# Kernel optimization log

Measured on AMD Instinct MI355X. Metric: run time of the kernel, lower is better.

Reference implementation:

```python
import jax, jax.numpy as jnp
import numpy as np

B, L, DIN, H, E, K = 64, 256, 768, 64, 8, 2
S = 16  # sqrt(L): token<->feature grid side
LOSS_COEF = 1e-2


def gelu(x):
    return jax.nn.gelu(x, approximate=False)  # torch nn.GELU (exact erf)


def cv_squared(v):
    v = v.astype(jnp.float32)
    return jnp.var(v, ddof=1) / (jnp.mean(v) ** 2 + 1e-10)


def setup_inputs() -> dict:
    key = jax.random.key(0)
    ks = jax.random.split(key, 16)
    rn = lambda k, shape, s=0.02: jax.random.normal(k, shape, jnp.float32) * s
    lap = jnp.array([[0., 1., 0.], [1., -4., 1.], [0., 1., 0.]], jnp.float32)
    return {
        "x": jax.random.normal(ks[0], (B, L, DIN), jnp.float32),
        "dte": jax.random.normal(ks[1], (B, L, DIN), jnp.float32),
        "w_gate": rn(ks[2], (L, E), 1.0),
        "W_exp": rn(ks[3], (E, DIN, H)), "b_exp": jnp.zeros((E, H), jnp.float32),
        "W_sh": rn(ks[4], (DIN, H)), "b_sh": jnp.zeros((H,), jnp.float32),
        "ln_g": jnp.ones((H,), jnp.float32), "ln_b": jnp.zeros((H,), jnp.float32),
        "W_px": rn(ks[5], (H, 2 * H)), "b_px": jnp.zeros((2 * H,), jnp.float32),
        "conv_sh": jnp.tile(lap[None, None], (H, 1, 1, 1)),  # depthwise Laplacian [H,1,3,3]
        "W_pxx": rn(ks[6], (H, H)), "b_pxx": jnp.zeros((H,), jnp.float32),
        "W_dte": rn(ks[7], (H, H)), "b_dte": jnp.zeros((H,), jnp.float32),
        "W_dteall": rn(ks[8], (H, H)), "b_dteall": jnp.zeros((H,), jnp.float32),
        "W_rgb": rn(ks[9], (DIN, H)), "b_rgb": jnp.zeros((H,), jnp.float32),
        "W_fx": rn(ks[10], (H, H)), "b_fx": jnp.zeros((H,), jnp.float32),
        "W_fmod": rn(ks[11], (H, H)), "b_fmod": jnp.zeros((H,), jnp.float32),
        "W_fxx": rn(ks[12], (H, H)), "b_fxx": jnp.zeros((H,), jnp.float32),
    }


def reference(x, dte, w_gate, W_exp, b_exp, W_sh, b_sh, ln_g, ln_b, W_px, b_px,
              conv_sh, W_pxx, b_pxx, W_dte, b_dte, W_dteall, b_dteall,
              W_rgb, b_rgb, W_fx, b_fx, W_fmod, b_fmod, W_fxx, b_fxx):
    # ---- top-k gating (clean logits; noisy_gating=False / eval) ----
    logits = dte.mean(-1) @ w_gate                     # [B,E]
    topv, topi = jax.lax.top_k(logits, K)
    topg = jax.nn.softmax(topv, axis=1)
    gates = jnp.zeros_like(logits).at[jnp.arange(B)[:, None], topi].set(topg)
    importance = gates.sum(0)
    load = (gates > 0).sum(0).astype(jnp.float32)
    loss = LOSS_COEF * (cv_squared(importance) + cv_squared(load))
    # ---- sparse dispatch / expert Linear / weighted combine (dense-equivalent) ----
    y = jnp.einsum('be,bld,edh->blh', gates, dte, W_exp) + (gates @ b_exp)[:, None, :]
    # ---- shared expert Linear + Shared block ----
    sh = dte @ W_sh + b_sh                             # [B,L,H]
    shortcut = sh
    t = (sh - sh.mean(-1, keepdims=True)) * jax.lax.rsqrt(sh.var(-1, keepdims=True) + 1e-6)
    t = t * ln_g + ln_b
    t = t @ W_px + b_px                                # [B,L,2H]
    t1, t2 = t[..., :H], t[..., H:]
    f = t1.transpose(0, 2, 1).reshape(B, H, S, S)      # token2feature
    f = jax.lax.conv_general_dilated(f, conv_sh, (1, 1), 'SAME', feature_group_count=H)
    t1 = f.reshape(B, H, L).transpose(0, 2, 1)         # feature2token
    sh = (gelu(t1) * t2) @ W_pxx + b_pxx + shortcut
    # ---- combine MoE and shared streams ----
    dte_tok = (y @ W_dte + b_dte) + (sh @ W_dteall + b_dteall)
    rgb_tok = x @ W_rgb + b_rgb
    # ---- Fusion (its self.norm was overwritten to GELU; token<->feature round-trip is identity) ----
    shortcut = rgb_tok
    a = gelu(rgb_tok) @ W_fx + b_fx
    m = gelu(dte_tok) @ W_fmod + b_fmod
    out = (gelu(m) * a) @ W_fxx + b_fxx + shortcut     # [B,L,H]
    return out, loss
```

## Files before the change

kernel.cpp:

```cpp
#include <hip/hip_runtime.h>
#include <math.h>

typedef unsigned short u16;
typedef unsigned int u32;
typedef __attribute__((ext_vector_type(8))) short bf16x8;
typedef __attribute__((ext_vector_type(4))) float f32x4;


__device__ __forceinline__ float bf2f(u16 u) {
    union { u32 i; float f; } x; x.i = ((u32)u) << 16; return x.f;
}
__device__ __forceinline__ u16 f2bf(float f) {
    union { float f; u32 i; } x; x.f = f;
    u32 i = x.i;
    return (u16)((i + 0x7fffu + ((i >> 16) & 1u)) >> 16);
}
__device__ __forceinline__ u32 pack2(float a, float b) {
    return (u32)f2bf(a) | ((u32)f2bf(b) << 16);
}
__device__ __forceinline__ float wsum(float v) {
    #pragma unroll
    for (int o = 1; o < 64; o <<= 1) v += __shfl_xor(v, o, 64);
    return v;
}
__device__ __forceinline__ float gelu_f(float x) {
    return 0.5f * x * (1.0f + erff(x * 0.70710678118654752440f));
}

__global__ __launch_bounds__(256) void k_gate_part(const float* __restrict__ dte,
                                                   const float* __restrict__ w_gate,
                                                   float* __restrict__ partial) {
    __shared__ float dmeanS[64];
    int p = blockIdx.x, tid = threadIdx.x, w = tid >> 6, lane = tid & 63;
    for (int i = 0; i < 16; i++) {
        int l = w * 16 + i;
        const float* pr = dte + ((size_t)p * 64 + l) * 768;
        float s = 0.f;
        #pragma unroll
        for (int j = 0; j < 3; j++) {
            float4 v = *(const float4*)(pr + (lane + j * 64) * 4);
            s += v.x + v.y + v.z + v.w;
        }
        s = wsum(s);
        if (lane == 0) dmeanS[l] = s * (1.f / 768.f);
    }
    __syncthreads();
    if (w == 0) {
        float dm = dmeanS[lane];
        int wl = (p & 3) * 64 + lane;
        #pragma unroll
        for (int e = 0; e < 8; e++) {
            float s = wsum(dm * w_gate[wl * 8 + e]);
            if (lane == 0) partial[p * 8 + e] = s;
        }
    }
}

__global__ __launch_bounds__(256) void k_gate_fin(const float* __restrict__ partial,
                                                  const float* __restrict__ b_exp,
                                                  int* __restrict__ topi,
                                                  float* __restrict__ topg,
                                                  float* __restrict__ bias_y,
                                                  float* __restrict__ loss_out) {
    __shared__ float gS[64 * 8];
    __shared__ int i0S[64], i1S[64];
    __shared__ float g0S[64], g1S[64];
    int tid = threadIdx.x;
    if (tid < 64) {
        float lg[8];
        #pragma unroll
        for (int e = 0; e < 8; e++)
            lg[e] = partial[(tid * 4 + 0) * 8 + e] + partial[(tid * 4 + 1) * 8 + e] +
                    partial[(tid * 4 + 2) * 8 + e] + partial[(tid * 4 + 3) * 8 + e];
        int i0 = 0; float v0 = lg[0];
        #pragma unroll
        for (int e = 1; e < 8; e++) if (lg[e] > v0) { v0 = lg[e]; i0 = e; }
        int i1 = -1; float v1 = -1e30f;
        #pragma unroll
        for (int e = 0; e < 8; e++) if (e != i0 && lg[e] > v1) { v1 = lg[e]; i1 = e; }
        if (i1 < 0) i1 = (i0 + 1) & 7;
        float e2 = expf(v1 - v0);
        float g0 = 1.f / (1.f + e2);
        float g1 = e2 / (1.f + e2);
        #pragma unroll
        for (int e = 0; e < 8; e++) gS[tid * 8 + e] = 0.f;
        gS[tid * 8 + i0] = g0;
        gS[tid * 8 + i1] = g1;
        i0S[tid] = i0; i1S[tid] = i1; g0S[tid] = g0; g1S[tid] = g1;
        topi[tid * 2] = i0; topi[tid * 2 + 1] = i1;
        topg[tid * 2] = g0; topg[tid * 2 + 1] = g1;
    }
    __syncthreads();
    for (int idx = tid; idx < 4096; idx += 256) {
        int b = idx >> 6, h = idx & 63;
        bias_y[idx] = g0S[b] * b_exp[i0S[b] * 64 + h] + g1S[b] * b_exp[i1S[b] * 64 + h];
    }
    if (tid < 64) {
        float g[8];
        #pragma unroll
        for (int e = 0; e < 8; e++) g[e] = gS[tid * 8 + e];
        float imp[8], ld[8];
        #pragma unroll
        for (int e = 0; e < 8; e++) {
            imp[e] = wsum(g[e]);
            ld[e]  = wsum(g[e] > 0.f ? 1.f : 0.f);
        }
        if (tid == 0) {
            float l = 0.f;
            {
                float s = 0.f;
                #pragma unroll
                for (int e = 0; e < 8; e++) s += imp[e];
                float mn = s / 8.f, v = 0.f;
                #pragma unroll
                for (int e = 0; e < 8; e++) { float d = imp[e] - mn; v += d * d; }
                l += (v / 7.f) / (mn * mn + 1e-10f);
            }
            {
                float s = 0.f;
                #pragma unroll
                for (int e = 0; e < 8; e++) s += ld[e];
                float mn = s / 8.f, v = 0.f;
                #pragma unroll
                for (int e = 0; e < 8; e++) { float d = ld[e] - mn; v += d * d; }
                l += (v / 7.f) / (mn * mn + 1e-10f);
            }
            loss_out[0] = 0.01f * l;
        }
    }
}

__global__ __launch_bounds__(256) void k_gemm3(const float* __restrict__ dte,
                                               const float* __restrict__ x,
                                               const float* __restrict__ W_sh,
                                               const float* __restrict__ b_sh,
                                               const float* __restrict__ W_exp,
                                               const int* __restrict__ topi,
                                               const float* __restrict__ topg,
                                               const float* __restrict__ bias_y,
                                               const float* __restrict__ W_rgb,
                                               const float* __restrict__ b_rgb,
                                               float* __restrict__ buf_sh,
                                               u16* __restrict__ buf_y,
                                               float* __restrict__ out_rgb) {
    __shared__ u16 As[64 * 40];
    __shared__ u16 Wt[64 * 40];
    int bid = blockIdx.x;
    int kind, row0;
    if (bid < 512) { kind = bid & 1; row0 = (bid >> 1) * 64; }
    else           { kind = 2;       row0 = (bid - 512) * 64; }
    int b = row0 >> 8;
    int tid = threadIdx.x, wv = tid >> 6, lane = tid & 63;
    int m = lane & 15, quad = lane >> 4;

    const float* A = (kind == 2) ? x : dte;
    const float* W0 = (kind == 2) ? W_rgb : W_sh;
    const float* W1 = W0;
    float g0 = 0.f, g1 = 0.f;
    if (kind == 1) {
        W0 = W_exp + (size_t)topi[2 * b] * 49152;
        W1 = W_exp + (size_t)topi[2 * b + 1] * 49152;
        g0 = topg[2 * b]; g1 = topg[2 * b + 1];
    }

    f32x4 acc0 = {0.f, 0.f, 0.f, 0.f}, acc1 = acc0, acc2 = acc0, acc3 = acc0;

    for (int kc = 0; kc < 24; kc++) {
        __syncthreads();
        #pragma unroll
        for (int j = 0; j < 2; j++) {
            int e4 = tid + j * 256;
            int r = e4 >> 3, kq = e4 & 7;
            float4 v = *(const float4*)(A + (size_t)(row0 + r) * 768 + kc * 32 + kq * 4);
            u32* d = (u32*)&As[r * 40 + kq * 4];
            d[0] = pack2(v.x, v.y);
            d[1] = pack2(v.z, v.w);
        }
        #pragma unroll
        for (int j = 0; j < 2; j++) {
            int e4 = tid + j * 256;
            int k = e4 >> 4, n4 = (e4 & 15) * 4;
            size_t off = (size_t)(kc * 32 + k) * 64 + n4;
            float4 wvv;
            if (kind == 1) {
                float4 a = *(const float4*)(W0 + off);
                float4 c = *(const float4*)(W1 + off);
                wvv.x = g0 * a.x + g1 * c.x; wvv.y = g0 * a.y + g1 * c.y;
                wvv.z = g0 * a.z + g1 * c.z; wvv.w = g0 * a.w + g1 * c.w;
            } else {
                wvv = *(const float4*)(W0 + off);
            }
            Wt[(n4 + 0) * 40 + k] = f2bf(wvv.x);
            Wt[(n4 + 1) * 40 + k] = f2bf(wvv.y);
            Wt[(n4 + 2) * 40 + k] = f2bf(wvv.z);
            Wt[(n4 + 3) * 40 + k] = f2bf(wvv.w);
        }
        __syncthreads();
        bf16x8 a = *(const bf16x8*)&As[(wv * 16 + m) * 40 + quad * 8];
        bf16x8 b0 = *(const bf16x8*)&Wt[(0 * 16 + m) * 40 + quad * 8];
        bf16x8 b1 = *(const bf16x8*)&Wt[(1 * 16 + m) * 40 + quad * 8];
        bf16x8 b2 = *(const bf16x8*)&Wt[(2 * 16 + m) * 40 + quad * 8];
        bf16x8 b3 = *(const bf16x8*)&Wt[(3 * 16 + m) * 40 + quad * 8];
        acc0 = __builtin_amdgcn_mfma_f32_16x16x32_bf16(a, b0, acc0, 0, 0, 0);
        acc1 = __builtin_amdgcn_mfma_f32_16x16x32_bf16(a, b1, acc1, 0, 0, 0);
        acc2 = __builtin_amdgcn_mfma_f32_16x16x32_bf16(a, b2, acc2, 0, 0, 0);
        acc3 = __builtin_amdgcn_mfma_f32_16x16x32_bf16(a, b3, acc3, 0, 0, 0);
    }

    f32x4 accs[4] = {acc0, acc1, acc2, acc3};
    #pragma unroll
    for (int t = 0; t < 4; t++) {
        int col = t * 16 + m;
        float bias;
        if (kind == 0)      bias = b_sh[col];
        else if (kind == 1) bias = bias_y[b * 64 + col];
        else                bias = b_rgb[col];
        #pragma unroll
        for (int i = 0; i < 4; i++) {
            int r = row0 + wv * 16 + quad * 4 + i;
            float val = accs[t][i] + bias;
            if (kind == 0)      buf_sh[(size_t)r * 64 + col] = val;
            else if (kind == 1) buf_y[(size_t)r * 64 + col] = f2bf(val);
            else                out_rgb[(size_t)r * 64 + col] = val;
        }
    }
}

__global__ __launch_bounds__(256) void k_lnpx(const float* __restrict__ buf_sh,
                                              const float* __restrict__ ln_g,
                                              const float* __restrict__ ln_b,
                                              const float* __restrict__ W_px,
                                              const float* __restrict__ b_px,
                                              u16* __restrict__ t1, u16* __restrict__ t2) {
    __shared__ float T[32 * 68];
    __shared__ float Wpx[8192];
    int r0 = blockIdx.x * 32;
    int tid = threadIdx.x, w = tid >> 6, lane = tid & 63;
    #pragma unroll
    for (int j = 0; j < 8; j++) {
        int e4 = tid + j * 256;
        *(float4*)(Wpx + e4 * 4) = *(const float4*)(W_px + e4 * 4);
    }
    float lnG = ln_g[lane], lnB = ln_b[lane];
    for (int i = 0; i < 8; i++) {
        int l = w * 8 + i;
        float v = buf_sh[(size_t)(r0 + l) * 64 + lane];
        float mean = wsum(v) * (1.f / 64.f);
        float d = v - mean;
        float var = wsum(d * d) * (1.f / 64.f);
        T[l * 68 + lane] = d * rsqrtf(var + 1e-6f) * lnG + lnB;
    }
    __syncthreads();
    int rg = tid >> 4, cg = tid & 15;
    float acc1[2][4] = {}, acc2[2][4] = {};
    const float* tr = T + rg * 2 * 68;
    #pragma unroll 4
    for (int kk = 0; kk < 64; kk++) {
        float a0 = tr[kk], a1 = tr[68 + kk];
        float4 w1 = *(const float4*)(Wpx + kk * 128 + cg * 4);
        float4 w2 = *(const float4*)(Wpx + kk * 128 + 64 + cg * 4);
        acc1[0][0] += a0 * w1.x; acc1[0][1] += a0 * w1.y; acc1[0][2] += a0 * w1.z; acc1[0][3] += a0 * w1.w;
        acc1[1][0] += a1 * w1.x; acc1[1][1] += a1 * w1.y; acc1[1][2] += a1 * w1.z; acc1[1][3] += a1 * w1.w;
        acc2[0][0] += a0 * w2.x; acc2[0][1] += a0 * w2.y; acc2[0][2] += a0 * w2.z; acc2[0][3] += a0 * w2.w;
        acc2[1][0] += a1 * w2.x; acc2[1][1] += a1 * w2.y; acc2[1][2] += a1 * w2.z; acc2[1][3] += a1 * w2.w;
    }
    float4 b1 = *(const float4*)(b_px + cg * 4);
    float4 b2 = *(const float4*)(b_px + 64 + cg * 4);
    #pragma unroll
    for (int i = 0; i < 2; i++) {
        int r = r0 + rg * 2 + i;
        u32* d1 = (u32*)(t1 + (size_t)r * 64 + cg * 4);
        d1[0] = pack2(acc1[i][0] + b1.x, acc1[i][1] + b1.y);
        d1[1] = pack2(acc1[i][2] + b1.z, acc1[i][3] + b1.w);
        u32* d2 = (u32*)(t2 + (size_t)r * 64 + cg * 4);
        d2[0] = pack2(acc2[i][0] + b2.x, acc2[i][1] + b2.y);
        d2[1] = pack2(acc2[i][2] + b2.z, acc2[i][3] + b2.w);
    }
}

__global__ __launch_bounds__(256) void k_tail(const u16* __restrict__ t1,
                                              const u16* __restrict__ t2,
                                              const float* __restrict__ conv_sh,
                                              const float* __restrict__ W_pxx,
                                              const float* __restrict__ b_pxx,
                                              const float* __restrict__ buf_sh,
                                              const u16* __restrict__ buf_y,
                                              const float* __restrict__ W_dte,
                                              const float* __restrict__ b_dte,
                                              const float* __restrict__ W_dteall,
                                              const float* __restrict__ b_dteall,
                                              const float* __restrict__ W_fx,
                                              const float* __restrict__ b_fx,
                                              const float* __restrict__ W_fmod,
                                              const float* __restrict__ b_fmod,
                                              const float* __restrict__ W_fxx,
                                              const float* __restrict__ b_fxx,
                                              float* __restrict__ out) {
    __shared__ float B0[32 * 68];
    __shared__ float B1[32 * 68];
    __shared__ float B2[32 * 68];
    __shared__ float RS[32 * 64];
    int r0 = blockIdx.x * 32;
    int tid = threadIdx.x, w = tid >> 6, lane = tid & 63;
    int rg = tid >> 4, cg = tid & 15;

    {
        float c0 = conv_sh[lane * 9 + 0], c1 = conv_sh[lane * 9 + 1], c2 = conv_sh[lane * 9 + 2];
        float c3 = conv_sh[lane * 9 + 3], c4 = conv_sh[lane * 9 + 4], c5 = conv_sh[lane * 9 + 5];
        float c6 = conv_sh[lane * 9 + 6], c7 = conv_sh[lane * 9 + 7], c8 = conv_sh[lane * 9 + 8];
        for (int i = 0; i < 8; i++) {
            int l = w * 8 + i;
            int gr = r0 + l;
            int pix = gr & 255, ii = pix >> 4, jj = pix & 15;
            const u16* p = t1 + (size_t)gr * 64 + lane;
            float c = c4 * bf2f(p[0]);
            if (ii > 0) {
                c += c1 * bf2f(p[-1024]);
                if (jj > 0)  c += c0 * bf2f(p[-1024 - 64]);
                if (jj < 15) c += c2 * bf2f(p[-1024 + 64]);
            }
            if (jj > 0)  c += c3 * bf2f(p[-64]);
            if (jj < 15) c += c5 * bf2f(p[64]);
            if (ii < 15) {
                c += c7 * bf2f(p[1024]);
                if (jj > 0)  c += c6 * bf2f(p[1024 - 64]);
                if (jj < 15) c += c8 * bf2f(p[1024 + 64]);
            }
            B0[l * 68 + lane] = gelu_f(c) * bf2f(t2[(size_t)gr * 64 + lane]);
        }
    }
    __syncthreads();

    {
        float acc[2][4] = {};
        const float* ur = B0 + rg * 2 * 68;
        #pragma unroll 8
        for (int kk = 0; kk < 64; kk++) {
            float a0 = ur[kk], a1 = ur[68 + kk];
            float4 wvv = *(const float4*)(W_pxx + kk * 64 + cg * 4);
            acc[0][0] += a0 * wvv.x; acc[0][1] += a0 * wvv.y; acc[0][2] += a0 * wvv.z; acc[0][3] += a0 * wvv.w;
            acc[1][0] += a1 * wvv.x; acc[1][1] += a1 * wvv.y; acc[1][2] += a1 * wvv.z; acc[1][3] += a1 * wvv.w;
        }
        float4 bp = *(const float4*)(b_pxx + cg * 4);
        #pragma unroll
        for (int i = 0; i < 2; i++) {
            int lr = rg * 2 + i;
            float4 shv = *(const float4*)(buf_sh + (size_t)(r0 + lr) * 64 + cg * 4);
            *(float4*)(B1 + lr * 68 + cg * 4) =
                make_float4(acc[i][0] + bp.x + shv.x, acc[i][1] + bp.y + shv.y,
                            acc[i][2] + bp.z + shv.z, acc[i][3] + bp.w + shv.w);
        }
    }
    __syncthreads();

    #pragma unroll
    for (int j = 0; j < 8; j++) {
        int e = tid + j * 256;
        int l = e >> 6, c = e & 63;
        B0[l * 68 + c] = bf2f(buf_y[(size_t)(r0 + l) * 64 + c]);
    }
    __syncthreads();

    {
        float acc[2][4] = {};
        const float* yr = B0 + rg * 2 * 68;
        const float* sr = B1 + rg * 2 * 68;
        #pragma unroll 4
        for (int kk = 0; kk < 64; kk++) {
            float y0 = yr[kk], y1 = yr[68 + kk];
            float s0 = sr[kk], s1 = sr[68 + kk];
            float4 w1 = *(const float4*)(W_dte + kk * 64 + cg * 4);
            float4 w2 = *(const float4*)(W_dteall + kk * 64 + cg * 4);
            acc[0][0] += y0 * w1.x + s0 * w2.x; acc[0][1] += y0 * w1.y + s0 * w2.y;
            acc[0][2] += y0 * w1.z + s0 * w2.z; acc[0][3] += y0 * w1.w + s0 * w2.w;
            acc[1][0] += y1 * w1.x + s1 * w2.x; acc[1][1] += y1 * w1.y + s1 * w2.y;
            acc[1][2] += y1 * w1.z + s1 * w2.z; acc[1][3] += y1 * w1.w + s1 * w2.w;
        }
        float4 bd1 = *(const float4*)(b_dte + cg * 4);
        float4 bd2 = *(const float4*)(b_dteall + cg * 4);
        #pragma unroll
        for (int i = 0; i < 2; i++) {
            int lr = rg * 2 + i;
            *(float4*)(B2 + lr * 68 + cg * 4) =
                make_float4(gelu_f(acc[i][0] + bd1.x + bd2.x), gelu_f(acc[i][1] + bd1.y + bd2.y),
                            gelu_f(acc[i][2] + bd1.z + bd2.z), gelu_f(acc[i][3] + bd1.w + bd2.w));
        }
    }
    __syncthreads();

    #pragma unroll
    for (int j = 0; j < 2; j++) {
        int e4 = tid + j * 256;
        int l = e4 >> 4, c4i = e4 & 15;
        float4 rv = *(const float4*)(out + (size_t)(r0 + l) * 64 + c4i * 4);
        *(float4*)(RS + l * 64 + c4i * 4) = rv;
        B1[l * 68 + c4i * 4 + 0] = gelu_f(rv.x);
        B1[l * 68 + c4i * 4 + 1] = gelu_f(rv.y);
        B1[l * 68 + c4i * 4 + 2] = gelu_f(rv.z);
        B1[l * 68 + c4i * 4 + 3] = gelu_f(rv.w);
    }
    __syncthreads();

    {
        float accA[2][4] = {}, accM[2][4] = {};
        const float* ga = B1 + rg * 2 * 68;
        const float* gm = B2 + rg * 2 * 68;
        #pragma unroll 4
        for (int kk = 0; kk < 64; kk++) {
            float a0 = ga[kk], a1 = ga[68 + kk];
            float m0 = gm[kk], m1 = gm[68 + kk];
            float4 wa = *(const float4*)(W_fx + kk * 64 + cg * 4);
            float4 wm = *(const float4*)(W_fmod + kk * 64 + cg * 4);
            accA[0][0] += a0 * wa.x; accA[0][1] += a0 * wa.y; accA[0][2] += a0 * wa.z; accA[0][3] += a0 * wa.w;
            accA[1][0] += a1 * wa.x; accA[1][1] += a1 * wa.y; accA[1][2] += a1 * wa.z; accA[1][3] += a1 * wa.w;
            accM[0][0] += m0 * wm.x; accM[0][1] += m0 * wm.y; accM[0][2] += m0 * wm.z; accM[0][3] += m0 * wm.w;
            accM[1][0] += m1 * wm.x; accM[1][1] += m1 * wm.y; accM[1][2] += m1 * wm.z; accM[1][3] += m1 * wm.w;
        }
        float4 bx = *(const float4*)(b_fx + cg * 4);
        float4 bm = *(const float4*)(b_fmod + cg * 4);
        #pragma unroll
        for (int i = 0; i < 2; i++) {
            int lr = rg * 2 + i;
            float a0 = accA[i][0] + bx.x, a1 = accA[i][1] + bx.y, a2 = accA[i][2] + bx.z, a3 = accA[i][3] + bx.w;
            float m0 = accM[i][0] + bm.x, m1 = accM[i][1] + bm.y, m2 = accM[i][2] + bm.z, m3 = accM[i][3] + bm.w;
            *(float4*)(B0 + lr * 68 + cg * 4) =
                make_float4(gelu_f(m0) * a0, gelu_f(m1) * a1, gelu_f(m2) * a2, gelu_f(m3) * a3);
        }
    }
    __syncthreads();

    {
        float acc[2][4] = {};
        const float* pr = B0 + rg * 2 * 68;
        #pragma unroll 8
        for (int kk = 0; kk < 64; kk++) {
            float p0 = pr[kk], p1 = pr[68 + kk];
            float4 wvv = *(const float4*)(W_fxx + kk * 64 + cg * 4);
            acc[0][0] += p0 * wvv.x; acc[0][1] += p0 * wvv.y; acc[0][2] += p0 * wvv.z; acc[0][3] += p0 * wvv.w;
            acc[1][0] += p1 * wvv.x; acc[1][1] += p1 * wvv.y; acc[1][2] += p1 * wvv.z; acc[1][3] += p1 * wvv.w;
        }
        float4 bo = *(const float4*)(b_fxx + cg * 4);
        #pragma unroll
        for (int i = 0; i < 2; i++) {
            int lr = rg * 2 + i;
            *(float4*)(out + (size_t)(r0 + lr) * 64 + cg * 4) =
                make_float4(acc[i][0] + bo.x + RS[lr * 64 + cg * 4 + 0],
                            acc[i][1] + bo.y + RS[lr * 64 + cg * 4 + 1],
                            acc[i][2] + bo.z + RS[lr * 64 + cg * 4 + 2],
                            acc[i][3] + bo.w + RS[lr * 64 + cg * 4 + 3]);
        }
    }
}

extern "C" void kernel_launch(void* const* d_in, const int* in_sizes, int n_in,
                              void* d_out, int out_size, void* d_ws, size_t ws_size,
                              hipStream_t stream) {
    const float* x       = (const float*)d_in[0];
    const float* dte     = (const float*)d_in[1];
    const float* w_gate  = (const float*)d_in[2];
    const float* W_exp   = (const float*)d_in[3];
    const float* b_exp   = (const float*)d_in[4];
    const float* W_sh    = (const float*)d_in[5];
    const float* b_sh    = (const float*)d_in[6];
    const float* ln_g    = (const float*)d_in[7];
    const float* ln_b    = (const float*)d_in[8];
    const float* W_px    = (const float*)d_in[9];
    const float* b_px    = (const float*)d_in[10];
    const float* conv_sh = (const float*)d_in[11];
    const float* W_pxx   = (const float*)d_in[12];
    const float* b_pxx   = (const float*)d_in[13];
    const float* W_dte   = (const float*)d_in[14];
    const float* b_dte   = (const float*)d_in[15];
    const float* W_dteall= (const float*)d_in[16];
    const float* b_dteall= (const float*)d_in[17];
    const float* W_rgb   = (const float*)d_in[18];
    const float* b_rgb   = (const float*)d_in[19];
    const float* W_fx    = (const float*)d_in[20];
    const float* b_fx    = (const float*)d_in[21];
    const float* W_fmod  = (const float*)d_in[22];
    const float* b_fmod  = (const float*)d_in[23];
    const float* W_fxx   = (const float*)d_in[24];
    const float* b_fxx   = (const float*)d_in[25];

    float* out = (float*)d_out;

    float* wsf    = (float*)d_ws;
    float* partial= wsf;
    int*   topi   = (int*)(wsf + 2048);
    float* topg   = wsf + 2176;
    float* bias_y = wsf + 2304;
    float* buf_sh = wsf + 8192;
    u16*   buf_y  = (u16*)(wsf + 8192 + 1048576);
    u16*   t1     = (u16*)(wsf + 8192 + 1048576 + 524288);
    u16*   t2     = (u16*)(wsf + 8192 + 1048576 + 524288*2);

    hipLaunchKernelGGL(k_gate_part, dim3(256), dim3(256), 0, stream, dte, w_gate, partial);
    hipLaunchKernelGGL(k_gate_fin, dim3(1), dim3(256), 0, stream,
                       partial, b_exp, topi, topg, bias_y, out + 1048576);
    hipLaunchKernelGGL(k_gemm3, dim3(768), dim3(256), 0, stream,
                       dte, x, W_sh, b_sh, W_exp, topi, topg, bias_y, W_rgb, b_rgb,
                       buf_sh, buf_y, out);
    hipLaunchKernelGGL(k_lnpx, dim3(512), dim3(256), 0, stream,
                       buf_sh, ln_g, ln_b, W_px, b_px, t1, t2);
    hipLaunchKernelGGL(k_tail, dim3(512), dim3(256), 0, stream,
                       t1, t2, conv_sh, W_pxx, b_pxx, buf_sh, buf_y,
                       W_dte, b_dte, W_dteall, b_dteall,
                       W_fx, b_fx, W_fmod, b_fmod, W_fxx, b_fxx, out);

    (void)in_sizes; (void)n_in; (void)out_size; (void)ws_size;
}
```

Baseline: 278.7 us.

## Prefetch next K-chunk into registers and double the K tile in gemm3

The main projection GEMM kernel now loads the next K chunk from global memory into registers while the MFMAs for the current chunk run, so global latency overlaps compute. The K tile grows from 32 to 64, which halves the number of barrier pairs, and the weight tile is now written transposed with 16-byte vector LDS stores instead of scalar stores. The cost is more registers per thread (prefetch buffers) and larger LDS tiles. The weight loads also become scalar but coalesced per column.

```diff
diff --git a/kernel.cpp b/kernel.cpp
--- a/kernel.cpp
+++ b/kernel.cpp
@@ -143,8 +143,8 @@
                                                float* __restrict__ buf_sh,
                                                u16* __restrict__ buf_y,
                                                float* __restrict__ out_rgb) {
-    __shared__ u16 As[64 * 40];
-    __shared__ u16 Wt[64 * 40];
+    __shared__ u16 As[64 * 72];
+    __shared__ u16 Wt[64 * 72];
     int bid = blockIdx.x;
     int kind, row0;
     if (bid < 512) { kind = bid & 1; row0 = (bid >> 1) * 64; }
@@ -163,48 +163,73 @@
         g0 = topg[2 * b]; g1 = topg[2 * b + 1];
     }
 
+    float4 pa[2][2];
+    float  pw[16];
+    const int a_r  = tid >> 3;
+    const int a_k8 = (tid & 7) * 8;
+    const int w_n  = tid & 63;
+    const int w_k0 = (tid >> 6) * 16;
+
+    auto loadA = [&](int kc) {
+        #pragma unroll
+        for (int j = 0; j < 2; j++) {
+            const float* src = A + (size_t)(row0 + a_r + j * 32) * 768 + kc * 64 + a_k8;
+            pa[j][0] = *(const float4*)(src);
+            pa[j][1] = *(const float4*)(src + 4);
+        }
+    };
+    auto loadW = [&](int kc) {
+        if (kind == 1) {
+            #pragma unroll
+            for (int j = 0; j < 16; j++) {
+                size_t off = (size_t)(kc * 64 + w_k0 + j) * 64 + w_n;
+                pw[j] = g0 * W0[off] + g1 * W1[off];
+            }
+        } else {
+            #pragma unroll
+            for (int j = 0; j < 16; j++)
+                pw[j] = W0[(size_t)(kc * 64 + w_k0 + j) * 64 + w_n];
+        }
+    };
+    auto stageLDS = [&]() {
+        #pragma unroll
+        for (int j = 0; j < 2; j++) {
+            uint4 d;
+            d.x = pack2(pa[j][0].x, pa[j][0].y);
+            d.y = pack2(pa[j][0].z, pa[j][0].w);
+            d.z = pack2(pa[j][1].x, pa[j][1].y);
+            d.w = pack2(pa[j][1].z, pa[j][1].w);
+            *(uint4*)&As[(a_r + j * 32) * 72 + a_k8] = d;
+        }
+        uint4 d0, d1;
+        d0.x = pack2(pw[0],  pw[1]);  d0.y = pack2(pw[2],  pw[3]);
+        d0.z = pack2(pw[4],  pw[5]);  d0.w = pack2(pw[6],  pw[7]);
+        d1.x = pack2(pw[8],  pw[9]);  d1.y = pack2(pw[10], pw[11]);
+        d1.z = pack2(pw[12], pw[13]); d1.w = pack2(pw[14], pw[15]);
+        *(uint4*)&Wt[w_n * 72 + w_k0]     = d0;
+        *(uint4*)&Wt[w_n * 72 + w_k0 + 8] = d1;
+    };
+
     f32x4 acc0 = {0.f, 0.f, 0.f, 0.f}, acc1 = acc0, acc2 = acc0, acc3 = acc0;
 
-    for (int kc = 0; kc < 24; kc++) {
+    loadA(0); loadW(0);
+    for (int kc = 0; kc < 12; kc++) {
         __syncthreads();
-        #pragma unroll
-        for (int j = 0; j < 2; j++) {
-            int e4 = tid + j * 256;
-            int r = e4 >> 3, kq = e4 & 7;
-            float4 v = *(const float4*)(A + (size_t)(row0 + r) * 768 + kc * 32 + kq * 4);
-            u32* d = (u32*)&As[r * 40 + kq * 4];
-            d[0] = pack2(v.x, v.y);
-            d[1] = pack2(v.z, v.w);
-        }
-        #pragma unroll
-        for (int j = 0; j < 2; j++) {
-            int e4 = tid + j * 256;
-            int k = e4 >> 4, n4 = (e4 & 15) * 4;
-            size_t off = (size_t)(kc * 32 + k) * 64 + n4;
-            float4 wvv;
-            if (kind == 1) {
-                float4 a = *(const float4*)(W0 + off);
-                float4 c = *(const float4*)(W1 + off);
-                wvv.x = g0 * a.x + g1 * c.x; wvv.y = g0 * a.y + g1 * c.y;
-                wvv.z = g0 * a.z + g1 * c.z; wvv.w = g0 * a.w + g1 * c.w;
-            } else {
-                wvv = *(const float4*)(W0 + off);
-            }
-            Wt[(n4 + 0) * 40 + k] = f2bf(wvv.x);
-            Wt[(n4 + 1) * 40 + k] = f2bf(wvv.y);
-            Wt[(n4 + 2) * 40 + k] = f2bf(wvv.z);
-            Wt[(n4 + 3) * 40 + k] = f2bf(wvv.w);
-        }
+        stageLDS();
         __syncthreads();
-        bf16x8 a = *(const bf16x8*)&As[(wv * 16 + m) * 40 + quad * 8];
-        bf16x8 b0 = *(const bf16x8*)&Wt[(0 * 16 + m) * 40 + quad * 8];
-        bf16x8 b1 = *(const bf16x8*)&Wt[(1 * 16 + m) * 40 + quad * 8];
-        bf16x8 b2 = *(const bf16x8*)&Wt[(2 * 16 + m) * 40 + quad * 8];
-        bf16x8 b3 = *(const bf16x8*)&Wt[(3 * 16 + m) * 40 + quad * 8];
-        acc0 = __builtin_amdgcn_mfma_f32_16x16x32_bf16(a, b0, acc0, 0, 0, 0);
-        acc1 = __builtin_amdgcn_mfma_f32_16x16x32_bf16(a, b1, acc1, 0, 0, 0);
-        acc2 = __builtin_amdgcn_mfma_f32_16x16x32_bf16(a, b2, acc2, 0, 0, 0);
-        acc3 = __builtin_amdgcn_mfma_f32_16x16x32_bf16(a, b3, acc3, 0, 0, 0);
+        if (kc < 11) { loadA(kc + 1); loadW(kc + 1); }
+        const int ar = (wv * 16 + m) * 72;
+        bf16x8 a0 = *(const bf16x8*)&As[ar + quad * 8];
+        bf16x8 a1 = *(const bf16x8*)&As[ar + 32 + quad * 8];
+        #pragma unroll
+        for (int t = 0; t < 4; t++) {
+            const int br = (t * 16 + m) * 72;
+            bf16x8 b0 = *(const bf16x8*)&Wt[br + quad * 8];
+            bf16x8 b1 = *(const bf16x8*)&Wt[br + 32 + quad * 8];
+            f32x4* accp = (t == 0) ? &acc0 : (t == 1) ? &acc1 : (t == 2) ? &acc2 : &acc3;
+            *accp = __builtin_amdgcn_mfma_f32_16x16x32_bf16(a0, b0, *accp, 0, 0, 0);
+            *accp = __builtin_amdgcn_mfma_f32_16x16x32_bf16(a1, b1, *accp, 0, 0, 0);
+        }
     }
 
     f32x4 accs[4] = {acc0, acc1, acc2, acc3};
```

After: 255.7 us. 1.09x faster.
